# Performance work log

Hardware: AMD Instinct MI355X
Metric: run time of the kernel (lower is better)

Reference implementation:

```python
import jax, jax.numpy as jnp
import numpy as np

N_SRC = 50000
N_DST = 50000
IN_FEATS = 256
OUT_FEATS = 32
NUM_HEADS = 4
N_EDGES = 800000


def setup_inputs() -> dict:
    key = jax.random.key(0)
    ks = jax.random.split(key, 7)
    h_src = jax.random.normal(ks[0], (N_SRC, IN_FEATS), dtype=jnp.float32)
    h_dst = jax.random.normal(ks[1], (N_DST, IN_FEATS), dtype=jnp.float32)
    # xavier-normal-ish scaling for the shared fc weight
    W = jax.random.normal(ks[2], (IN_FEATS, NUM_HEADS * OUT_FEATS), dtype=jnp.float32) * (
        jnp.sqrt(2.0) * jnp.sqrt(2.0 / (IN_FEATS + NUM_HEADS * OUT_FEATS))
    )
    attn_l = jax.random.normal(ks[3], (NUM_HEADS, OUT_FEATS), dtype=jnp.float32) * 0.1
    attn_r = jax.random.normal(ks[4], (NUM_HEADS, OUT_FEATS), dtype=jnp.float32) * 0.1
    src_idx = jax.random.randint(ks[5], (N_EDGES,), 0, N_SRC, dtype=jnp.int32)
    dst_idx = jax.random.randint(ks[6], (N_EDGES,), 0, N_DST, dtype=jnp.int32)
    return {"h_src": h_src, "h_dst": h_dst, "W": W, "attn_l": attn_l,
            "attn_r": attn_r, "src_idx": src_idx, "dst_idx": dst_idx}


def reference(h_src, h_dst, W, attn_l, attn_r, src_idx, dst_idx):
    H, F = NUM_HEADS, OUT_FEATS
    # shared linear projection (no bias), reshape to [N, H, F]
    ft_src = (h_src @ W).reshape(-1, H, F)            # [N_src, H, F]
    ft_dst = (h_dst @ W).reshape(-1, H, F)            # [N_dst, H, F]
    # per-node attention logits, [N, H]
    el = jnp.einsum('nhf,hf->nh', ft_src, attn_l)
    er = jnp.einsum('nhf,hf->nh', ft_dst, attn_r)
    # u_add_v gather over edges, LeakyReLU(0.2) -> [E, H]
    e = jax.nn.leaky_relu(el[src_idx] + er[dst_idx], negative_slope=0.2)
    # edge softmax over incoming edges of each destination node
    smax = jax.ops.segment_max(e, dst_idx, num_segments=N_DST)   # [N_dst, H]
    e_exp = jnp.exp(e - smax[dst_idx])                           # [E, H]
    ssum = jax.ops.segment_sum(e_exp, dst_idx, num_segments=N_DST)
    a = e_exp / ssum[dst_idx]                                    # [E, H]
    # u_mul_e + scatter-sum aggregation -> [N_dst, H, F]
    msg = ft_src[src_idx] * a[:, :, None]
    rst = jax.ops.segment_sum(msg, dst_idx, num_segments=N_DST)
    return rst
```

## Files before the change

### kernel.cpp

```cpp
#include <hip/hip_runtime.h>

#define IN_FEATS 256
#define OUT_FEATS 32
#define NUM_HEADS 4
#define NHF 128

typedef __attribute__((ext_vector_type(8))) short short8;
typedef __attribute__((ext_vector_type(4))) float f32x4;

__device__ inline unsigned short f2bf(float f) {
    unsigned int u = __builtin_bit_cast(unsigned int, f);
    u = (u + 0x7fff + ((u >> 16) & 1)) >> 16;
    return (unsigned short)u;
}
__device__ inline float bfhi2f(unsigned int packed_hi) {
    return __builtin_bit_cast(float, packed_hi);
}

__global__ __launch_bounds__(256) void prep(const float* __restrict__ W,
                                            const float* __restrict__ attn_r,
                                            float* __restrict__ v,
                                            unsigned short* __restrict__ Wt,
                                            int* __restrict__ bcnt) {
    if (blockIdx.x < 128) {
        int n = blockIdx.x;
        int k = threadIdx.x;
        Wt[n * 256 + k] = f2bf(W[(size_t)k * NHF + n]);
    } else {
        bcnt[threadIdx.x] = 0;
        for (int p = threadIdx.x; p < IN_FEATS * NUM_HEADS; p += 256) {
            int k = p >> 2, h = p & 3;
            const float* wr = W + (size_t)k * NHF + h * OUT_FEATS;
            const float* ar = attn_r + h * OUT_FEATS;
            float s = 0.f;
            #pragma unroll
            for (int f = 0; f < OUT_FEATS; ++f) s += wr[f] * ar[f];
            v[p] = s;
        }
    }
}

#define BSTRIDE 136
__global__ __launch_bounds__(256) void gemm_el(const float* __restrict__ A,
                                               const unsigned short* __restrict__ Wt,
                                               const float* __restrict__ attn_l,
                                               unsigned short* __restrict__ ft16,
                                               float* __restrict__ el, int M) {
    __shared__ unsigned short WtL[128 * 256];

    const int wave = threadIdx.x >> 6;
    const int lane = threadIdx.x & 63;
    const int quad = lane >> 4;
    const int mc   = lane & 15;
    const int row_base = blockIdx.x * 64 + wave * 16;

    for (int i = threadIdx.x; i < 4096; i += 256) {
        const int n = i >> 5, c = i & 31;
        const int cs = (c + n) & 31;
        *(uint4*)(WtL + n * 256 + cs * 8) = *(const uint4*)(Wt + n * 256 + c * 8);
    }

    float al[8];
    #pragma unroll
    for (int t = 0; t < 8; ++t) al[t] = attn_l[(t >> 1) * 32 + (t & 1) * 16 + mc];

    const int rowA = min(row_base + mc, M - 1);
    const float* arow = A + (size_t)rowA * IN_FEATS;

    float4 a[8][2];
    #pragma unroll
    for (int kk = 0; kk < 8; ++kk) {
        a[kk][0] = *(const float4*)(arow + kk * 32 + quad * 8);
        a[kk][1] = *(const float4*)(arow + kk * 32 + quad * 8 + 4);
    }

    f32x4 acc[8];
    #pragma unroll
    for (int t = 0; t < 8; ++t) acc[t] = (f32x4){0.f, 0.f, 0.f, 0.f};

    __syncthreads();

    #pragma unroll
    for (int kk = 0; kk < 8; ++kk) {
        short8 af;
        af[0] = (short)f2bf(a[kk][0].x); af[1] = (short)f2bf(a[kk][0].y);
        af[2] = (short)f2bf(a[kk][0].z); af[3] = (short)f2bf(a[kk][0].w);
        af[4] = (short)f2bf(a[kk][1].x); af[5] = (short)f2bf(a[kk][1].y);
        af[6] = (short)f2bf(a[kk][1].z); af[7] = (short)f2bf(a[kk][1].w);
        #pragma unroll
        for (int t = 0; t < 8; ++t) {
            const int n = t * 16 + mc;
            const int c = ((kk << 2) + quad + n) & 31;
            const short8 bf = *(const short8*)(WtL + n * 256 + c * 8);
            acc[t] = __builtin_amdgcn_mfma_f32_16x16x32_bf16(af, bf, acc[t], 0, 0, 0);
        }
    }

    float elp[4][4];
    #pragma unroll
    for (int v = 0; v < 4; ++v)
        #pragma unroll
        for (int h = 0; h < 4; ++h) elp[v][h] = 0.f;
    #pragma unroll
    for (int v = 0; v < 4; ++v)
        #pragma unroll
        for (int t = 0; t < 8; ++t) elp[v][t >> 1] += acc[t][v] * al[t];
    #pragma unroll
    for (int v = 0; v < 4; ++v)
        #pragma unroll
        for (int h = 0; h < 4; ++h) {
            #pragma unroll
            for (int d = 1; d < 16; d <<= 1)
                elp[v][h] += __shfl_xor(elp[v][h], d, 64);
        }

    #pragma unroll
    for (int v = 0; v < 4; ++v) {
        const int rg = row_base + quad * 4 + v;
        if (rg < M && mc < 4) {
            float ev = (mc == 0) ? elp[v][0] : (mc == 1) ? elp[v][1]
                     : (mc == 2) ? elp[v][2] : elp[v][3];
            el[(size_t)rg * 4 + mc] = ev;
        }
    }

    __syncthreads();
    #pragma unroll
    for (int v = 0; v < 4; ++v) {
        const int lr = wave * 16 + quad * 4 + v;
        #pragma unroll
        for (int t = 0; t < 8; ++t)
            WtL[lr * BSTRIDE + t * 16 + mc] = f2bf(acc[t][v]);
    }
    __syncthreads();
    const int rows_in_blk = min(64, M - blockIdx.x * 64);
    for (int i = threadIdx.x; i < 64 * 16; i += 256) {
        const int lr = i >> 4, seg = i & 15;
        if (lr < rows_in_blk)
            *(uint4*)(ft16 + (size_t)(blockIdx.x * 64 + lr) * NHF + seg * 8) =
                *(const uint4*)(WtL + lr * BSTRIDE + seg * 8);
    }
}

__global__ __launch_bounds__(256) void compute_er(const float* __restrict__ hdst,
                                                  const float* __restrict__ v,
                                                  float* __restrict__ er, int M) {
    int wid  = (blockIdx.x * blockDim.x + threadIdx.x) >> 6;
    int lane = threadIdx.x & 63;
    if (wid >= M) return;
    const float4 x = *(const float4*)(hdst + (size_t)wid * IN_FEATS + lane * 4);
    const float4* vp = (const float4*)(v + (size_t)lane * 16);
    float4 v0 = vp[0], v1 = vp[1], v2 = vp[2], v3 = vp[3];
    float a0 = x.x * v0.x + x.y * v1.x + x.z * v2.x + x.w * v3.x;
    float a1 = x.x * v0.y + x.y * v1.y + x.z * v2.y + x.w * v3.y;
    float a2 = x.x * v0.z + x.y * v1.z + x.z * v2.z + x.w * v3.z;
    float a3 = x.x * v0.w + x.y * v1.w + x.z * v2.w + x.w * v3.w;
    #pragma unroll
    for (int m = 32; m >= 1; m >>= 1) {
        a0 += __shfl_xor(a0, m, 64);
        a1 += __shfl_xor(a1, m, 64);
        a2 += __shfl_xor(a2, m, 64);
        a3 += __shfl_xor(a3, m, 64);
    }
    if (lane == 0) *(float4*)(er + (size_t)wid * 4) = make_float4(a0, a1, a2, a3);
}


__global__ __launch_bounds__(256) void bucket_hist(const int* __restrict__ dst,
                                                   int* __restrict__ bcnt, int E) {
    __shared__ int h[256];
    h[threadIdx.x] = 0;
    __syncthreads();
    for (int e = blockIdx.x * 256 + threadIdx.x; e < E; e += gridDim.x * 256)
        atomicAdd(&h[dst[e] >> 8], 1);
    __syncthreads();
    int c = h[threadIdx.x];
    if (c) atomicAdd(&bcnt[threadIdx.x], c);
}

__global__ __launch_bounds__(256) void bucket_scan(const int* __restrict__ bcnt,
                                                   int* __restrict__ bbase,
                                                   int* __restrict__ bcursor,
                                                   int* __restrict__ off, int n_dst, int E) {
    __shared__ int s[256];
    int t = threadIdx.x;
    int v = bcnt[t];
    s[t] = v;
    __syncthreads();
    #pragma unroll
    for (int d = 1; d < 256; d <<= 1) {
        int x = (t >= d) ? s[t - d] : 0;
        __syncthreads();
        s[t] += x;
        __syncthreads();
    }
    int ex = s[t] - v;
    bbase[t] = ex;
    bcursor[t] = ex;
    if (t == 255) bbase[256] = s[255];
    if (t == 0) off[n_dst] = E;
}

__global__ __launch_bounds__(256) void bin_pairs(const int* __restrict__ src,
                                                 const int* __restrict__ dst,
                                                 int* __restrict__ bcursor,
                                                 unsigned int* __restrict__ pairs, int E) {
    __shared__ int cnt[256];
    __shared__ int basel[256];
    const int e0 = blockIdx.x * 4096;
    const int e1 = min(e0 + 4096, E);
    const int t = threadIdx.x;
    cnt[t] = 0;
    __syncthreads();
    for (int e = e0 + t; e < e1; e += 256)
        atomicAdd(&cnt[dst[e] >> 8], 1);
    __syncthreads();
    int c = cnt[t];
    basel[t] = c ? atomicAdd(&bcursor[t], c) : 0;
    __syncthreads();
    cnt[t] = 0;
    __syncthreads();
    for (int e = e0 + t; e < e1; e += 256) {
        int d = dst[e];
        int b = d >> 8;
        int o = atomicAdd(&cnt[b], 1);
        pairs[basel[b] + o] = (unsigned int)src[e] | ((unsigned int)(d & 255) << 16);
    }
}

__global__ __launch_bounds__(256) void fine_csr(const unsigned int* __restrict__ pairs,
                                                const int* __restrict__ bbase,
                                                int* __restrict__ off,
                                                int* __restrict__ csr_src, int n_dst) {
    __shared__ int cnt[256];
    __shared__ int cur[256];
    const int b = blockIdx.x;
    const int p0 = bbase[b], p1 = bbase[b + 1];
    const int t = threadIdx.x;
    cnt[t] = 0;
    __syncthreads();
    for (int p = p0 + t; p < p1; p += 256)
        atomicAdd(&cnt[pairs[p] >> 16], 1);
    __syncthreads();
    int v = cnt[t];
    cur[t] = v;
    __syncthreads();
    #pragma unroll
    for (int d = 1; d < 256; d <<= 1) {
        int x = (t >= d) ? cur[t - d] : 0;
        __syncthreads();
        cur[t] += x;
        __syncthreads();
    }
    int ex = cur[t] - v;
    int node = b * 256 + t;
    if (node < n_dst) off[node] = p0 + ex;
    __syncthreads();
    cur[t] = ex;
    __syncthreads();
    for (int p = p0 + t; p < p1; p += 256) {
        unsigned int pr = pairs[p];
        int o = atomicAdd(&cur[pr >> 16], 1);
        csr_src[p0 + o] = (int)(pr & 0xffffu);
    }
}

__global__ __launch_bounds__(256) void agg_pull(const int* __restrict__ off,
                                                const int* __restrict__ csr_src,
                                                const float* __restrict__ el,
                                                const float* __restrict__ er,
                                                const uint2* __restrict__ ftp,
                                                float* __restrict__ out, int n_dst) {
    const int wid  = (blockIdx.x * blockDim.x + threadIdx.x) >> 6;
    const int lane = threadIdx.x & 63;
    const int half = lane >> 5;
    const int hl   = lane & 31;
    const int node = wid * 2 + half;
    const bool valid = node < n_dst;
    const int nc = valid ? node : 0;
    const int h  = hl >> 3;
    const float er_h = er[nc * 4 + h];
    const int start = off[nc];
    const int end   = valid ? off[nc + 1] : start;
    const int deg   = end - start;
    const int last  = max(end - 1, 0);

    const int sl = csr_src[min(start + hl, last)];

    const int mdeg  = max(deg, __shfl_xor(deg, 32, 64));
    const int iters = (min(mdeg, 32) + 7) >> 3;

    float a0 = 0.f, a1 = 0.f, a2 = 0.f, a3 = 0.f, sw = 0.f;

    float e[8]; uint2 q[8];
    #pragma unroll
    for (int j = 0; j < 8; ++j) {
        const int s = __shfl(sl, j, 32);
        e[j] = el[s * 4 + h];
        q[j] = ftp[s * 32 + hl];
    }

    for (int i = 0; i < iters; ++i) {
        float f[8]; uint2 r[8];
        const int jn = (i + 1) << 3;
        #pragma unroll
        for (int j = 0; j < 8; ++j) {
            const int s = __shfl(sl, min(jn + j, 31), 32);
            f[j] = el[s * 4 + h];
            r[j] = ftp[s * 32 + hl];
        }

        const int kb = start + (i << 3);
        #pragma unroll
        for (int j = 0; j < 8; ++j) {
            float x = e[j] + er_h;
            x = fmaxf(x, 0.2f * x);
            const float w = (kb + j < end) ? __expf(x) : 0.f;
            sw += w;
            a0 = fmaf(bfhi2f(q[j].x << 16),          w, a0);
            a1 = fmaf(bfhi2f(q[j].x & 0xffff0000u),  w, a1);
            a2 = fmaf(bfhi2f(q[j].y << 16),          w, a2);
            a3 = fmaf(bfhi2f(q[j].y & 0xffff0000u),  w, a3);
        }

        #pragma unroll
        for (int j = 0; j < 8; ++j) { e[j] = f[j]; q[j] = r[j]; }
    }

    for (int k = start + 32; k < end; ++k) {
        const int s = csr_src[k];
        float x = el[s * 4 + h] + er_h;
        x = fmaxf(x, 0.2f * x);
        const float w = __expf(x);
        const uint2 qq = ftp[s * 32 + hl];
        sw += w;
        a0 = fmaf(bfhi2f(qq.x << 16),         w, a0);
        a1 = fmaf(bfhi2f(qq.x & 0xffff0000u), w, a1);
        a2 = fmaf(bfhi2f(qq.y << 16),         w, a2);
        a3 = fmaf(bfhi2f(qq.y & 0xffff0000u), w, a3);
    }

    if (valid) {
        const float inv = (deg > 0) ? 1.f / sw : 0.f;
        float4 r;
        r.x = a0 * inv; r.y = a1 * inv; r.z = a2 * inv; r.w = a3 * inv;
        *(float4*)(out + (size_t)node * NHF + hl * 4) = r;
    }
}

extern "C" void kernel_launch(void* const* d_in, const int* in_sizes, int n_in,
                              void* d_out, int out_size, void* d_ws, size_t ws_size,
                              hipStream_t stream) {
    const float* h_src  = (const float*)d_in[0];
    const float* h_dst  = (const float*)d_in[1];
    const float* W      = (const float*)d_in[2];
    const float* attn_l = (const float*)d_in[3];
    const float* attn_r = (const float*)d_in[4];
    const int* src_idx  = (const int*)d_in[5];
    const int* dst_idx  = (const int*)d_in[6];

    const int n_src = in_sizes[0] / IN_FEATS;
    const int n_dst = in_sizes[1] / IN_FEATS;
    const int E     = in_sizes[5];

    const int nbuck = (n_dst + 255) >> 8;

    char* ws = (char*)d_ws;
    size_t o = 0;
    float* v       = (float*)(ws + o); o += 4096;
    float* el      = (float*)(ws + o); o += (size_t)n_src * 4 * sizeof(float);
    float* er      = (float*)(ws + o); o += (size_t)n_dst * 4 * sizeof(float);
    int*   off     = (int*)(ws + o);   o += ((size_t)n_dst + 16) * sizeof(int);
    int*   bcnt    = (int*)(ws + o);   o += 256 * sizeof(int);
    int*   bbase   = (int*)(ws + o);   o += 260 * sizeof(int);
    int*   bcursor = (int*)(ws + o);   o += 256 * sizeof(int);
    unsigned short* Wt = (unsigned short*)(ws + o); o += (size_t)NHF * IN_FEATS * sizeof(unsigned short);
    int*   csr_src = (int*)(ws + o);   o += (size_t)E * sizeof(int);
    unsigned int* pairs = (unsigned int*)(ws + o); o += (size_t)E * sizeof(unsigned int);
    unsigned short* ft16 = (unsigned short*)(ws + o); o += (size_t)n_src * NHF * sizeof(unsigned short);

    float* out = (float*)d_out;

    prep<<<129, 256, 0, stream>>>(W, attn_r, v, Wt, bcnt);
    gemm_el<<<(n_src + 63) / 64, 256, 0, stream>>>(h_src, Wt, attn_l, ft16, el, n_src);
    compute_er<<<(n_dst + 3) / 4, 256, 0, stream>>>(h_dst, v, er, n_dst);
    bucket_hist<<<512, 256, 0, stream>>>(dst_idx, bcnt, E);
    bucket_scan<<<1, 256, 0, stream>>>(bcnt, bbase, bcursor, off, n_dst, E);
    bin_pairs<<<(E + 4095) / 4096, 256, 0, stream>>>(src_idx, dst_idx, bcursor, pairs, E);
    fine_csr<<<nbuck, 256, 0, stream>>>(pairs, bbase, off, csr_src, n_dst);
    {
        const int nwave = (n_dst + 1) >> 1;
        agg_pull<<<(nwave + 3) / 4, 256, 0, stream>>>(off, csr_src, el, er,
                                                      (const uint2*)ft16, out, n_dst);
    }
}
```

Baseline: 255.0 us.

## Fuse CSR build stages into fewer launches with deterministic per-block partial histograms

Merges the weight prep with the bucket histogram, replaces global atomic cursors with per-block partial histograms that each bin_pairs block prefix-sums itself, and folds the fine CSR build into the GEMM launch as extra blocks. Launches drop from eight to five, cutting launch gaps and serial single-block kernels. In exchange, each block redundantly scans a 196x256 partial table, and bin_pairs now uses only 196 blocks with large edge chunks, which lowers parallelism in that stage.

```diff
diff --git a/kernel.cpp b/kernel.cpp
--- a/kernel.cpp
+++ b/kernel.cpp
@@ -17,18 +17,19 @@
     return __builtin_bit_cast(float, packed_hi);
 }
 
-__global__ __launch_bounds__(256) void prep(const float* __restrict__ W,
-                                            const float* __restrict__ attn_r,
-                                            float* __restrict__ v,
-                                            unsigned short* __restrict__ Wt,
-                                            int* __restrict__ bcnt) {
-    if (blockIdx.x < 128) {
-        int n = blockIdx.x;
-        int k = threadIdx.x;
-        Wt[n * 256 + k] = f2bf(W[(size_t)k * NHF + n]);
-    } else {
-        bcnt[threadIdx.x] = 0;
-        for (int p = threadIdx.x; p < IN_FEATS * NUM_HEADS; p += 256) {
+__global__ __launch_bounds__(256) void prep_hist(const float* __restrict__ W,
+                                                 const float* __restrict__ attn_r,
+                                                 const int* __restrict__ dst,
+                                                 float* __restrict__ v,
+                                                 unsigned short* __restrict__ Wt,
+                                                 int* __restrict__ partial,
+                                                 int nb, int E) {
+    const int t = threadIdx.x;
+    const int b = blockIdx.x;
+    if (b < 128) {
+        Wt[b * 256 + t] = f2bf(W[(size_t)t * NHF + b]);
+    } else if (b == 128) {
+        for (int p = t; p < IN_FEATS * NUM_HEADS; p += 256) {
             int k = p >> 2, h = p & 3;
             const float* wr = W + (size_t)k * NHF + h * OUT_FEATS;
             const float* ar = attn_r + h * OUT_FEATS;
@@ -37,108 +38,58 @@
             for (int f = 0; f < OUT_FEATS; ++f) s += wr[f] * ar[f];
             v[p] = s;
         }
-    }
-}
-
-#define BSTRIDE 136
-__global__ __launch_bounds__(256) void gemm_el(const float* __restrict__ A,
-                                               const unsigned short* __restrict__ Wt,
-                                               const float* __restrict__ attn_l,
-                                               unsigned short* __restrict__ ft16,
-                                               float* __restrict__ el, int M) {
-    __shared__ unsigned short WtL[128 * 256];
-
-    const int wave = threadIdx.x >> 6;
-    const int lane = threadIdx.x & 63;
-    const int quad = lane >> 4;
-    const int mc   = lane & 15;
-    const int row_base = blockIdx.x * 64 + wave * 16;
-
-    for (int i = threadIdx.x; i < 4096; i += 256) {
-        const int n = i >> 5, c = i & 31;
-        const int cs = (c + n) & 31;
-        *(uint4*)(WtL + n * 256 + cs * 8) = *(const uint4*)(Wt + n * 256 + c * 8);
-    }
-
-    float al[8];
-    #pragma unroll
-    for (int t = 0; t < 8; ++t) al[t] = attn_l[(t >> 1) * 32 + (t & 1) * 16 + mc];
-
-    const int rowA = min(row_base + mc, M - 1);
-    const float* arow = A + (size_t)rowA * IN_FEATS;
-
-    float4 a[8][2];
-    #pragma unroll
-    for (int kk = 0; kk < 8; ++kk) {
-        a[kk][0] = *(const float4*)(arow + kk * 32 + quad * 8);
-        a[kk][1] = *(const float4*)(arow + kk * 32 + quad * 8 + 4);
-    }
-
-    f32x4 acc[8];
-    #pragma unroll
-    for (int t = 0; t < 8; ++t) acc[t] = (f32x4){0.f, 0.f, 0.f, 0.f};
-
+    } else {
+        __shared__ int cnt[256];
+        const int hb = b - 129;
+        const int chunk = (E + nb - 1) / nb;
+        const int e0 = hb * chunk;
+        const int e1 = min(e0 + chunk, E);
+        cnt[t] = 0;
+        __syncthreads();
+        for (int e = e0 + t; e < e1; e += 256)
+            atomicAdd(&cnt[dst[e] >> 8], 1);
+        __syncthreads();
+        partial[hb * 256 + t] = cnt[t];
+    }
+}
+
+__global__ __launch_bounds__(256) void bin_pairs(const int* __restrict__ src,
+                                                 const int* __restrict__ dst,
+                                                 const int* __restrict__ partial,
+                                                 unsigned int* __restrict__ pairs,
+                                                 int nb, int E) {
+    __shared__ int sc[256];
+    __shared__ int basel[256];
+    __shared__ int cnt[256];
+    const int t = threadIdx.x;
+    const int b = blockIdx.x;
+    const int chunk = (E + nb - 1) / nb;
+    const int e0 = b * chunk;
+    const int e1 = min(e0 + chunk, E);
+
+    int colsum = 0, rowpref = 0;
+    for (int bb = 0; bb < nb; ++bb) {
+        const int pv = partial[bb * 256 + t];
+        colsum += pv;
+        if (bb < b) rowpref += pv;
+    }
+    sc[t] = colsum;
     __syncthreads();
-
-    #pragma unroll
-    for (int kk = 0; kk < 8; ++kk) {
-        short8 af;
-        af[0] = (short)f2bf(a[kk][0].x); af[1] = (short)f2bf(a[kk][0].y);
-        af[2] = (short)f2bf(a[kk][0].z); af[3] = (short)f2bf(a[kk][0].w);
-        af[4] = (short)f2bf(a[kk][1].x); af[5] = (short)f2bf(a[kk][1].y);
-        af[6] = (short)f2bf(a[kk][1].z); af[7] = (short)f2bf(a[kk][1].w);
-        #pragma unroll
-        for (int t = 0; t < 8; ++t) {
-            const int n = t * 16 + mc;
-            const int c = ((kk << 2) + quad + n) & 31;
-            const short8 bf = *(const short8*)(WtL + n * 256 + c * 8);
-            acc[t] = __builtin_amdgcn_mfma_f32_16x16x32_bf16(af, bf, acc[t], 0, 0, 0);
-        }
-    }
-
-    float elp[4][4];
-    #pragma unroll
-    for (int v = 0; v < 4; ++v)
-        #pragma unroll
-        for (int h = 0; h < 4; ++h) elp[v][h] = 0.f;
-    #pragma unroll
-    for (int v = 0; v < 4; ++v)
-        #pragma unroll
-        for (int t = 0; t < 8; ++t) elp[v][t >> 1] += acc[t][v] * al[t];
-    #pragma unroll
-    for (int v = 0; v < 4; ++v)
-        #pragma unroll
-        for (int h = 0; h < 4; ++h) {
-            #pragma unroll
-            for (int d = 1; d < 16; d <<= 1)
-                elp[v][h] += __shfl_xor(elp[v][h], d, 64);
-        }
-
-    #pragma unroll
-    for (int v = 0; v < 4; ++v) {
-        const int rg = row_base + quad * 4 + v;
-        if (rg < M && mc < 4) {
-            float ev = (mc == 0) ? elp[v][0] : (mc == 1) ? elp[v][1]
-                     : (mc == 2) ? elp[v][2] : elp[v][3];
-            el[(size_t)rg * 4 + mc] = ev;
-        }
-    }
-
+    #pragma unroll
+    for (int d = 1; d < 256; d <<= 1) {
+        int x = (t >= d) ? sc[t - d] : 0;
+        __syncthreads();
+        sc[t] += x;
+        __syncthreads();
+    }
+    basel[t] = (sc[t] - colsum) + rowpref;
+    cnt[t] = 0;
     __syncthreads();
-    #pragma unroll
-    for (int v = 0; v < 4; ++v) {
-        const int lr = wave * 16 + quad * 4 + v;
-        #pragma unroll
-        for (int t = 0; t < 8; ++t)
-            WtL[lr * BSTRIDE + t * 16 + mc] = f2bf(acc[t][v]);
-    }
-    __syncthreads();
-    const int rows_in_blk = min(64, M - blockIdx.x * 64);
-    for (int i = threadIdx.x; i < 64 * 16; i += 256) {
-        const int lr = i >> 4, seg = i & 15;
-        if (lr < rows_in_blk)
-            *(uint4*)(ft16 + (size_t)(blockIdx.x * 64 + lr) * NHF + seg * 8) =
-                *(const uint4*)(WtL + lr * BSTRIDE + seg * 8);
+    for (int e = e0 + t; e < e1; e += 256) {
+        int d = dst[e];
+        int bk = d >> 8;
+        int o = atomicAdd(&cnt[bk], 1);
+        pairs[basel[bk] + o] = (unsigned int)src[e] | ((unsigned int)(d & 255) << 16);
     }
 }
 
@@ -165,103 +116,162 @@
     if (lane == 0) *(float4*)(er + (size_t)wid * 4) = make_float4(a0, a1, a2, a3);
 }
 
-
-__global__ __launch_bounds__(256) void bucket_hist(const int* __restrict__ dst,
-                                                   int* __restrict__ bcnt, int E) {
-    __shared__ int h[256];
-    h[threadIdx.x] = 0;
+#define BSTRIDE 136
+__global__ __launch_bounds__(256) void gemm_fine(const float* __restrict__ A,
+                                                 const unsigned short* __restrict__ Wt,
+                                                 const float* __restrict__ attn_l,
+                                                 unsigned short* __restrict__ ft16,
+                                                 float* __restrict__ el, int M,
+                                                 const unsigned int* __restrict__ pairs,
+                                                 const int* __restrict__ partial,
+                                                 int* __restrict__ off,
+                                                 int* __restrict__ csr_src,
+                                                 int nb, int n_dst, int E) {
+    __shared__ unsigned short WtL[128 * 256];
+
+    if (blockIdx.x < (unsigned)nb) {
+        int* cnt = (int*)WtL;
+        int* cur = (int*)WtL + 256;
+        int* sc  = (int*)WtL + 512;
+        const int t = threadIdx.x;
+        const int b = blockIdx.x;
+
+        int colsum = 0;
+        for (int bb = 0; bb < nb; ++bb) colsum += partial[bb * 256 + t];
+        sc[t] = colsum;
+        __syncthreads();
+        #pragma unroll
+        for (int d = 1; d < 256; d <<= 1) {
+            int x = (t >= d) ? sc[t - d] : 0;
+            __syncthreads();
+            sc[t] += x;
+            __syncthreads();
+        }
+        const int p1 = sc[b];
+        const int p0 = (b == 0) ? 0 : sc[b - 1];
+
+        cnt[t] = 0;
+        __syncthreads();
+        for (int p = p0 + t; p < p1; p += 256)
+            atomicAdd(&cnt[pairs[p] >> 16], 1);
+        __syncthreads();
+        int vv = cnt[t];
+        cur[t] = vv;
+        __syncthreads();
+        #pragma unroll
+        for (int d = 1; d < 256; d <<= 1) {
+            int x = (t >= d) ? cur[t - d] : 0;
+            __syncthreads();
+            cur[t] += x;
+            __syncthreads();
+        }
+        int ex = cur[t] - vv;
+        int node = b * 256 + t;
+        if (node < n_dst) off[node] = p0 + ex;
+        if (b == 0 && t == 0) off[n_dst] = E;
+        __syncthreads();
+        cur[t] = ex;
+        __syncthreads();
+        for (int p = p0 + t; p < p1; p += 256) {
+            unsigned int pr = pairs[p];
+            int o = atomicAdd(&cur[pr >> 16], 1);
+            csr_src[p0 + o] = (int)(pr & 0xffffu);
+        }
+        return;
+    }
+
+    const int gb   = blockIdx.x - nb;
+    const int wave = threadIdx.x >> 6;
+    const int lane = threadIdx.x & 63;
+    const int quad = lane >> 4;
+    const int mc   = lane & 15;
+    const int row_base = gb * 64 + wave * 16;
+
+    for (int i = threadIdx.x; i < 4096; i += 256) {
+        const int n = i >> 5, c = i & 31;
+        const int cs = (c + n) & 31;
+        *(uint4*)(WtL + n * 256 + cs * 8) = *(const uint4*)(Wt + n * 256 + c * 8);
+    }
+
+    float al[8];
+    #pragma unroll
+    for (int t = 0; t < 8; ++t) al[t] = attn_l[(t >> 1) * 32 + (t & 1) * 16 + mc];
+
+    const int rowA = min(row_base + mc, M - 1);
+    const float* arow = A + (size_t)rowA * IN_FEATS;
+
+    float4 a[8][2];
+    #pragma unroll
+    for (int kk = 0; kk < 8; ++kk) {
+        a[kk][0] = *(const float4*)(arow + kk * 32 + quad * 8);
+        a[kk][1] = *(const float4*)(arow + kk * 32 + quad * 8 + 4);
+    }
+
+    f32x4 acc[8];
+    #pragma unroll
+    for (int t = 0; t < 8; ++t) acc[t] = (f32x4){0.f, 0.f, 0.f, 0.f};
+
     __syncthreads();
-    for (int e = blockIdx.x * 256 + threadIdx.x; e < E; e += gridDim.x * 256)
-        atomicAdd(&h[dst[e] >> 8], 1);
+
+    #pragma unroll
+    for (int kk = 0; kk < 8; ++kk) {
+        short8 af;
+        af[0] = (short)f2bf(a[kk][0].x); af[1] = (short)f2bf(a[kk][0].y);
+        af[2] = (short)f2bf(a[kk][0].z); af[3] = (short)f2bf(a[kk][0].w);
+        af[4] = (short)f2bf(a[kk][1].x); af[5] = (short)f2bf(a[kk][1].y);
+        af[6] = (short)f2bf(a[kk][1].z); af[7] = (short)f2bf(a[kk][1].w);
+        #pragma unroll
+        for (int t = 0; t < 8; ++t) {
+            const int n = t * 16 + mc;
+            const int c = ((kk << 2) + quad + n) & 31;
+            const short8 bf = *(const short8*)(WtL + n * 256 + c * 8);
+            acc[t] = __builtin_amdgcn_mfma_f32_16x16x32_bf16(af, bf, acc[t], 0, 0, 0);
+        }
+    }
+
+    float elp[4][4];
+    #pragma unroll
+    for (int v = 0; v < 4; ++v)
+        #pragma unroll
+        for (int h = 0; h < 4; ++h) elp[v][h] = 0.f;
+    #pragma unroll
+    for (int v = 0; v < 4; ++v)
+        #pragma unroll
+        for (int t = 0; t < 8; ++t) elp[v][t >> 1] += acc[t][v] * al[t];
+    #pragma unroll
+    for (int v = 0; v < 4; ++v)
+        #pragma unroll
+        for (int h = 0; h < 4; ++h) {
+            #pragma unroll
+            for (int d = 1; d < 16; d <<= 1)
+                elp[v][h] += __shfl_xor(elp[v][h], d, 64);
+        }
+
+    #pragma unroll
+    for (int v = 0; v < 4; ++v) {
+        const int rg = row_base + quad * 4 + v;
+        if (rg < M && mc < 4) {
+            float ev = (mc == 0) ? elp[v][0] : (mc == 1) ? elp[v][1]
+                     : (mc == 2) ? elp[v][2] : elp[v][3];
+            el[(size_t)rg * 4 + mc] = ev;
+        }
+    }
+
     __syncthreads();
-    int c = h[threadIdx.x];
-    if (c) atomicAdd(&bcnt[threadIdx.x], c);
-}
-
-__global__ __launch_bounds__(256) void bucket_scan(const int* __restrict__ bcnt,
-                                                   int* __restrict__ bbase,
-                                                   int* __restrict__ bcursor,
-                                                   int* __restrict__ off, int n_dst, int E) {
-    __shared__ int s[256];
-    int t = threadIdx.x;
-    int v = bcnt[t];
-    s[t] = v;
+    #pragma unroll
+    for (int v = 0; v < 4; ++v) {
+        const int lr = wave * 16 + quad * 4 + v;
+        #pragma unroll
+        for (int t = 0; t < 8; ++t)
+            WtL[lr * BSTRIDE + t * 16 + mc] = f2bf(acc[t][v]);
+    }
     __syncthreads();
-    #pragma unroll
-    for (int d = 1; d < 256; d <<= 1) {
-        int x = (t >= d) ? s[t - d] : 0;
-        __syncthreads();
-        s[t] += x;
-        __syncthreads();
-    }
-    int ex = s[t] - v;
-    bbase[t] = ex;
-    bcursor[t] = ex;
-    if (t == 255) bbase[256] = s[255];
-    if (t == 0) off[n_dst] = E;
-}
-
-__global__ __launch_bounds__(256) void bin_pairs(const int* __restrict__ src,
-                                                 const int* __restrict__ dst,
-                                                 int* __restrict__ bcursor,
-                                                 unsigned int* __restrict__ pairs, int E) {
-    __shared__ int cnt[256];
-    __shared__ int basel[256];
-    const int e0 = blockIdx.x * 4096;
-    const int e1 = min(e0 + 4096, E);
-    const int t = threadIdx.x;
-    cnt[t] = 0;
-    __syncthreads();
-    for (int e = e0 + t; e < e1; e += 256)
-        atomicAdd(&cnt[dst[e] >> 8], 1);
-    __syncthreads();
-    int c = cnt[t];
-    basel[t] = c ? atomicAdd(&bcursor[t], c) : 0;
-    __syncthreads();
-    cnt[t] = 0;
-    __syncthreads();
-    for (int e = e0 + t; e < e1; e += 256) {
-        int d = dst[e];
-        int b = d >> 8;
-        int o = atomicAdd(&cnt[b], 1);
-        pairs[basel[b] + o] = (unsigned int)src[e] | ((unsigned int)(d & 255) << 16);
-    }
-}
-
-__global__ __launch_bounds__(256) void fine_csr(const unsigned int* __restrict__ pairs,
-                                                const int* __restrict__ bbase,
-                                                int* __restrict__ off,
-                                                int* __restrict__ csr_src, int n_dst) {
-    __shared__ int cnt[256];
-    __shared__ int cur[256];
-    const int b = blockIdx.x;
-    const int p0 = bbase[b], p1 = bbase[b + 1];
-    const int t = threadIdx.x;
-    cnt[t] = 0;
-    __syncthreads();
-    for (int p = p0 + t; p < p1; p += 256)
-        atomicAdd(&cnt[pairs[p] >> 16], 1);
-    __syncthreads();
-    int v = cnt[t];
-    cur[t] = v;
-    __syncthreads();
-    #pragma unroll
-    for (int d = 1; d < 256; d <<= 1) {
-        int x = (t >= d) ? cur[t - d] : 0;
-        __syncthreads();
-        cur[t] += x;
-        __syncthreads();
-    }
-    int ex = cur[t] - v;
-    int node = b * 256 + t;
-    if (node < n_dst) off[node] = p0 + ex;
-    __syncthreads();
-    cur[t] = ex;
-    __syncthreads();
-    for (int p = p0 + t; p < p1; p += 256) {
-        unsigned int pr = pairs[p];
-        int o = atomicAdd(&cur[pr >> 16], 1);
-        csr_src[p0 + o] = (int)(pr & 0xffffu);
+    const int rows_in_blk = min(64, M - gb * 64);
+    for (int i = threadIdx.x; i < 64 * 16; i += 256) {
+        const int lr = i >> 4, seg = i & 15;
+        if (lr < rows_in_blk)
+            *(uint4*)(ft16 + (size_t)(gb * 64 + lr) * NHF + seg * 8) =
+                *(const uint4*)(WtL + lr * BSTRIDE + seg * 8);
     }
 }
 
@@ -363,7 +373,7 @@
     const int n_dst = in_sizes[1] / IN_FEATS;
     const int E     = in_sizes[5];
 
-    const int nbuck = (n_dst + 255) >> 8;
+    const int nb = (n_dst + 255) >> 8;
 
     char* ws = (char*)d_ws;
     size_t o = 0;
@@ -371,9 +381,7 @@
     float* el      = (float*)(ws + o); o += (size_t)n_src * 4 * sizeof(float);
     float* er      = (float*)(ws + o); o += (size_t)n_dst * 4 * sizeof(float);
     int*   off     = (int*)(ws + o);   o += ((size_t)n_dst + 16) * sizeof(int);
-    int*   bcnt    = (int*)(ws + o);   o += 256 * sizeof(int);
-    int*   bbase   = (int*)(ws + o);   o += 260 * sizeof(int);
-    int*   bcursor = (int*)(ws + o);   o += 256 * sizeof(int);
+    int*   partial = (int*)(ws + o);   o += 256 * 256 * sizeof(int);
     unsigned short* Wt = (unsigned short*)(ws + o); o += (size_t)NHF * IN_FEATS * sizeof(unsigned short);
     int*   csr_src = (int*)(ws + o);   o += (size_t)E * sizeof(int);
     unsigned int* pairs = (unsigned int*)(ws + o); o += (size_t)E * sizeof(unsigned int);
@@ -381,13 +389,12 @@
 
     float* out = (float*)d_out;
 
-    prep<<<129, 256, 0, stream>>>(W, attn_r, v, Wt, bcnt);
-    gemm_el<<<(n_src + 63) / 64, 256, 0, stream>>>(h_src, Wt, attn_l, ft16, el, n_src);
+    prep_hist<<<129 + nb, 256, 0, stream>>>(W, attn_r, dst_idx, v, Wt, partial, nb, E);
+    bin_pairs<<<nb, 256, 0, stream>>>(src_idx, dst_idx, partial, pairs, nb, E);
     compute_er<<<(n_dst + 3) / 4, 256, 0, stream>>>(h_dst, v, er, n_dst);
-    bucket_hist<<<512, 256, 0, stream>>>(dst_idx, bcnt, E);
-    bucket_scan<<<1, 256, 0, stream>>>(bcnt, bbase, bcursor, off, n_dst, E);
-    bin_pairs<<<(E + 4095) / 4096, 256, 0, stream>>>(src_idx, dst_idx, bcursor, pairs, E);
-    fine_csr<<<nbuck, 256, 0, stream>>>(pairs, bbase, off, csr_src, n_dst);
+    gemm_fine<<<nb + (n_src + 63) / 64, 256, 0, stream>>>(h_src, Wt, attn_l, ft16, el,
+                                                          n_src, pairs, partial, off,
+                                                          csr_src, nb, n_dst, E);
     {
         const int nwave = (n_dst + 1) >> 1;
         agg_pull<<<(nwave + 3) / 4, 256, 0, stream>>>(off, csr_src, el, er,
```

Result: no change. 258.1 us (+1.2%).
